# Optimization experiments

Measured on AMD Instinct MI355X. Metric: run time of the kernel, lower is better.

The kernel has to match this reference:

```python
import jax, jax.numpy as jnp
import numpy as np

N_NODES = 50000
N_EDGES = 600000
D_IN = 128
D_HID = 128
D_OUT = 40
EPS = 1e-5


def setup_inputs() -> dict:
    key = jax.random.key(0)
    ks = jax.random.split(key, 16)
    inp = {
        "x": jax.random.normal(ks[0], (N_NODES, D_IN), dtype=jnp.float32),
        "edge_index": jax.random.randint(ks[1], (2, N_EDGES), 0, N_NODES, dtype=jnp.int64),
    }
    dims = [(D_IN, D_HID), (D_HID, D_HID), (D_HID, D_OUT)]
    for i, (di, do) in enumerate(dims):
        s = 1.0 / np.sqrt(di)
        inp[f"W_l{i}"] = jax.random.uniform(ks[2 + 3 * i], (di, do), jnp.float32, -s, s)
        inp[f"b_l{i}"] = jax.random.uniform(ks[3 + 3 * i], (do,), jnp.float32, -s, s)
        inp[f"W_r{i}"] = jax.random.uniform(ks[4 + 3 * i], (di, do), jnp.float32, -s, s)
    for i in range(2):  # num_convs - 1 Trans (LayerNorm) blocks
        inp[f"g{i}"] = jnp.ones((D_HID,), jnp.float32)
        inp[f"be{i}"] = jnp.zeros((D_HID,), jnp.float32)
    return inp


def _sage_conv(x, src, dst, W_l, b_l, W_r):
    # mean-aggregate neighbor features at dst, then lin_l(agg) + lin_r(x)
    msg = jax.ops.segment_sum(x[src], dst, num_segments=N_NODES)  # [N, d]
    deg = jax.ops.segment_sum(jnp.ones((src.shape[0],), x.dtype), dst, num_segments=N_NODES)
    agg = msg / jnp.clip(deg, 1.0)[:, None]
    return agg @ W_l + b_l + x @ W_r


def _trans(x, g, b):
    # LayerNorm -> GELU (exact); Dropout p=0 is identity
    mu = jnp.mean(x, axis=-1, keepdims=True)
    var = jnp.mean(jnp.square(x - mu), axis=-1, keepdims=True)
    xn = (x - mu) * jax.lax.rsqrt(var + EPS) * g + b
    return jax.nn.gelu(xn, approximate=False)


def reference(x, edge_index, W_l0, b_l0, W_r0, W_l1, b_l1, W_r1, W_l2, b_l2, W_r2, g0, be0, g1, be1):
    src, dst = edge_index[0], edge_index[1]
    h = _sage_conv(x, src, dst, W_l0, b_l0, W_r0)
    h = _sage_conv(_trans(h, g0, be0), src, dst, W_l1, b_l1, W_r1)
    h = _sage_conv(_trans(h, g1, be1), src, dst, W_l2, b_l2, W_r2)
    return jax.nn.log_softmax(h, axis=1)
```

## Files before the change

kernel.cpp:

```cpp
#include <hip/hip_runtime.h>
#include <math.h>

#define N_NODES 50000
#define N_EDGES 600000
#define DF 128
#define KK 256
#define DOUT 40
#define EPSN 1e-5f
#define NB1 196

typedef __attribute__((ext_vector_type(8))) short sh8;
typedef __attribute__((ext_vector_type(4))) float f32x4;

__device__ __forceinline__ unsigned short f2b(float f) {
  unsigned u = __builtin_bit_cast(unsigned, f);
  unsigned r = u + 0x7FFFu + ((u >> 16) & 1u);
  return (unsigned short)(r >> 16);
}
__device__ __forceinline__ float b2f(unsigned short b) {
  unsigned u = ((unsigned)b) << 16;
  return __builtin_bit_cast(float, u);
}

__global__ __launch_bounds__(256) void k_count(
    const int* __restrict__ ei, int* __restrict__ counts) {
  int e = blockIdx.x * 256 + threadIdx.x;
  if (e < N_EDGES) atomicAdd(&counts[ei[N_EDGES + e]], 1);
}

__global__ __launch_bounds__(256) void k_bsum(
    const int* __restrict__ counts, int* __restrict__ bsum) {
  int i = blockIdx.x * 256 + threadIdx.x;
  int v = (i < N_NODES) ? counts[i] : 0;
  #pragma unroll
  for (int m = 1; m < 64; m <<= 1) v += __shfl_xor(v, m);
  __shared__ int ws[4];
  if ((threadIdx.x & 63) == 0) ws[threadIdx.x >> 6] = v;
  __syncthreads();
  if (threadIdx.x == 0) bsum[blockIdx.x] = ws[0] + ws[1] + ws[2] + ws[3];
}

__global__ __launch_bounds__(256) void k_bscan(
    const int* __restrict__ bsum, int* __restrict__ bbase) {
  const int t = threadIdx.x, lane = t & 63, w = t >> 6;
  int v = (t < NB1) ? bsum[t] : 0;
  int s = v;
  #pragma unroll
  for (int off = 1; off < 64; off <<= 1) {
    int u = __shfl_up(s, off);
    if (lane >= off) s += u;
  }
  __shared__ int wtot[4];
  if (lane == 63) wtot[w] = s;
  __syncthreads();
  int add = 0;
  for (int k = 0; k < w; ++k) add += wtot[k];
  if (t < NB1) bbase[t] = s + add - v;
}

__global__ __launch_bounds__(256) void k_rowptr(
    const int* __restrict__ counts, const int* __restrict__ bbase,
    int* __restrict__ rowptr, int* __restrict__ cursor,
    float* __restrict__ invdeg) {
  const int i = blockIdx.x * 256 + threadIdx.x;
  const int lane = threadIdx.x & 63, w = threadIdx.x >> 6;
  int c = (i < N_NODES) ? counts[i] : 0;
  int s = c;
  #pragma unroll
  for (int off = 1; off < 64; off <<= 1) {
    int u = __shfl_up(s, off);
    if (lane >= off) s += u;
  }
  __shared__ int wtot[4];
  if (lane == 63) wtot[w] = s;
  __syncthreads();
  int add = bbase[blockIdx.x];
  for (int k = 0; k < w; ++k) add += wtot[k];
  if (i < N_NODES) {
    int excl = s - c + add;
    rowptr[i] = excl;
    cursor[i] = excl;
    invdeg[i] = 1.0f / (float)((c > 1) ? c : 1);
  }
  if (i == 0) rowptr[N_NODES] = N_EDGES;
}

__global__ __launch_bounds__(256) void k_fill(
    const int* __restrict__ ei, int* __restrict__ cursor, int* __restrict__ csr) {
  int e = blockIdx.x * 256 + threadIdx.x;
  if (e < N_EDGES) {
    int d = ei[N_EDGES + e];
    int p = atomicAdd(&cursor[d], 1);
    csr[p] = ei[e];
  }
}

__global__ __launch_bounds__(256) void k_cvt_x(
    const float* __restrict__ x, unsigned* __restrict__ A) {
  int i = blockIdx.x * 256 + threadIdx.x;
  if (i >= N_NODES * 64) return;
  int n = i >> 6, p = i & 63;
  float2 v = ((const float2*)x)[i];
  A[(size_t)n * 128 + 64 + p] = (unsigned)f2b(v.x) | ((unsigned)f2b(v.y) << 16);
}

__global__ __launch_bounds__(256) void k_cvt_w(
    const float* __restrict__ Wl, const float* __restrict__ Wr,
    unsigned short* __restrict__ WT, int Nact, int total) {
  int i = blockIdx.x * 256 + threadIdx.x;
  if (i >= total) return;
  int n = i >> 8, k = i & 255;
  float v = 0.0f;
  if (n < Nact) v = (k < DF) ? Wl[k * Nact + n] : Wr[(k - DF) * Nact + n];
  WT[i] = f2b(v);
}

__global__ __launch_bounds__(256) void k_agg(
    unsigned* __restrict__ A, const int* __restrict__ rowptr,
    const int* __restrict__ csr, const float* __restrict__ invdeg) {
  const int node = (blockIdx.x * 256 + threadIdx.x) >> 6;
  const int lane = threadIdx.x & 63;
  if (node >= N_NODES) return;
  const int beg = rowptr[node], end = rowptr[node + 1];
  float ax = 0.f, ay = 0.f, bx = 0.f, by = 0.f;
  float cx = 0.f, cy = 0.f, dx = 0.f, dy = 0.f;
  int j = beg;
  for (; j + 4 <= end; j += 4) {
    int c0 = csr[j], c1 = csr[j + 1], c2 = csr[j + 2], c3 = csr[j + 3];
    unsigned p0 = A[(size_t)c0 * 128 + 64 + lane];
    unsigned p1 = A[(size_t)c1 * 128 + 64 + lane];
    unsigned p2 = A[(size_t)c2 * 128 + 64 + lane];
    unsigned p3 = A[(size_t)c3 * 128 + 64 + lane];
    ax += b2f((unsigned short)p0); ay += b2f((unsigned short)(p0 >> 16));
    bx += b2f((unsigned short)p1); by += b2f((unsigned short)(p1 >> 16));
    cx += b2f((unsigned short)p2); cy += b2f((unsigned short)(p2 >> 16));
    dx += b2f((unsigned short)p3); dy += b2f((unsigned short)(p3 >> 16));
  }
  for (; j < end; ++j) {
    unsigned p = A[(size_t)csr[j] * 128 + 64 + lane];
    ax += b2f((unsigned short)p); ay += b2f((unsigned short)(p >> 16));
  }
  ax += bx + cx + dx;
  ay += by + cy + dy;
  const float rd = invdeg[node];
  A[(size_t)node * 128 + lane] =
      (unsigned)f2b(ax * rd) | ((unsigned)f2b(ay * rd) << 16);
}

__global__ __launch_bounds__(256) void k_gemm128(
    const unsigned short* __restrict__ Acat, const unsigned short* __restrict__ WT,
    const float* __restrict__ bl, const float* __restrict__ g,
    const float* __restrict__ be, unsigned short* __restrict__ Adst) {
  __shared__ unsigned short Wlds[128 * KK];
  const int t = threadIdx.x;
  #pragma unroll
  for (int it = 0; it < 16; ++it) {
    int c = it * 256 + t;
    int n = c >> 5, k16 = c & 31;
    sh8 v = *(const sh8*)(WT + (size_t)n * KK + k16 * 8);
    unsigned off = (unsigned)((n * 512 + k16 * 16) ^ ((n & 7) << 4));
    *(sh8*)((char*)Wlds + off) = v;
  }
  __syncthreads();

  const int wave = t >> 6, lane = t & 63;
  const int lr = lane & 15, lg = lane >> 4;
  const int rw = blockIdx.x * 128 + wave * 32;

  sh8 a[2][8];
  #pragma unroll
  for (int rf = 0; rf < 2; ++rf) {
    int arow = rw + rf * 16 + lr;
    if (arow >= N_NODES) arow = N_NODES - 1;
    const sh8* Ap = (const sh8*)(Acat + (size_t)arow * KK + lg * 8);
    #pragma unroll
    for (int ks = 0; ks < 8; ++ks) a[rf][ks] = Ap[ks * 4];
  }

  f32x4 accs[2][8];
  #pragma unroll
  for (int rf = 0; rf < 2; ++rf)
    #pragma unroll
    for (int f = 0; f < 8; ++f) accs[rf][f] = (f32x4){0.f, 0.f, 0.f, 0.f};

  #pragma unroll
  for (int f = 0; f < 8; ++f) {
    const int n = f * 16 + lr;
    const unsigned swz = (unsigned)((n & 7) << 4);
    #pragma unroll
    for (int ks = 0; ks < 8; ++ks) {
      unsigned off = (unsigned)(n * 512 + ks * 64 + lg * 16) ^ swz;
      sh8 b = *(const sh8*)((const char*)Wlds + off);
      accs[0][f] = __builtin_amdgcn_mfma_f32_16x16x32_bf16(a[0][ks], b, accs[0][f], 0, 0, 0);
      accs[1][f] = __builtin_amdgcn_mfma_f32_16x16x32_bf16(a[1][ks], b, accs[1][f], 0, 0, 0);
    }
  }

  #pragma unroll
  for (int rf = 0; rf < 2; ++rf) {
    float s[4] = {0, 0, 0, 0}, sq[4] = {0, 0, 0, 0};
    #pragma unroll
    for (int f = 0; f < 8; ++f) {
      float bc = bl[lr + 16 * f];
      #pragma unroll
      for (int r = 0; r < 4; ++r) {
        float v = accs[rf][f][r] + bc;
        accs[rf][f][r] = v;
        s[r] += v; sq[r] += v * v;
      }
    }
    #pragma unroll
    for (int m = 1; m < 16; m <<= 1) {
      #pragma unroll
      for (int r = 0; r < 4; ++r) {
        s[r]  += __shfl_xor(s[r], m);
        sq[r] += __shfl_xor(sq[r], m);
      }
    }
    #pragma unroll
    for (int r = 0; r < 4; ++r) {
      float mu = s[r] * (1.0f / 128.0f);
      float var = sq[r] * (1.0f / 128.0f) - mu * mu;
      float rs = rsqrtf(var + EPSN);
      s[r] = mu; sq[r] = rs;
    }
    #pragma unroll
    for (int f = 0; f < 8; ++f) {
      float gv = g[lr + 16 * f], bev = be[lr + 16 * f];
      #pragma unroll
      for (int r = 0; r < 4; ++r) {
        int row = rw + rf * 16 + lg * 4 + r;
        float xn = (accs[rf][f][r] - s[r]) * sq[r] * gv + bev;
        float gel = 0.5f * xn * (1.0f + erff(xn * 0.70710678118654752f));
        if (row < N_NODES)
          Adst[(size_t)row * KK + 128 + lr + 16 * f] = f2b(gel);
      }
    }
  }
}

__global__ __launch_bounds__(256) void k_gemm40(
    const unsigned short* __restrict__ Acat, const unsigned short* __restrict__ WT,
    const float* __restrict__ bl, float* __restrict__ out) {
  __shared__ unsigned short Wlds[48 * KK];
  const int t = threadIdx.x;
  #pragma unroll
  for (int it = 0; it < 6; ++it) {
    int c = it * 256 + t;
    int n = c >> 5, k16 = c & 31;
    sh8 v = *(const sh8*)(WT + (size_t)n * KK + k16 * 8);
    unsigned off = (unsigned)((n * 512 + k16 * 16) ^ ((n & 7) << 4));
    *(sh8*)((char*)Wlds + off) = v;
  }
  __syncthreads();

  const int wave = t >> 6, lane = t & 63;
  const int lr = lane & 15, lg = lane >> 4;
  const int rw = blockIdx.x * 128 + wave * 32;

  sh8 a[2][8];
  #pragma unroll
  for (int rf = 0; rf < 2; ++rf) {
    int arow = rw + rf * 16 + lr;
    if (arow >= N_NODES) arow = N_NODES - 1;
    const sh8* Ap = (const sh8*)(Acat + (size_t)arow * KK + lg * 8);
    #pragma unroll
    for (int ks = 0; ks < 8; ++ks) a[rf][ks] = Ap[ks * 4];
  }

  f32x4 accs[2][3];
  #pragma unroll
  for (int rf = 0; rf < 2; ++rf)
    #pragma unroll
    for (int f = 0; f < 3; ++f) accs[rf][f] = (f32x4){0.f, 0.f, 0.f, 0.f};

  #pragma unroll
  for (int f = 0; f < 3; ++f) {
    const int n = f * 16 + lr;
    const unsigned swz = (unsigned)((n & 7) << 4);
    #pragma unroll
    for (int ks = 0; ks < 8; ++ks) {
      unsigned off = (unsigned)(n * 512 + ks * 64 + lg * 16) ^ swz;
      sh8 b = *(const sh8*)((const char*)Wlds + off);
      accs[0][f] = __builtin_amdgcn_mfma_f32_16x16x32_bf16(a[0][ks], b, accs[0][f], 0, 0, 0);
      accs[1][f] = __builtin_amdgcn_mfma_f32_16x16x32_bf16(a[1][ks], b, accs[1][f], 0, 0, 0);
    }
  }

  const bool v2 = (lr < 8);
  #pragma unroll
  for (int rf = 0; rf < 2; ++rf) {
    float vals[3][4];
    #pragma unroll
    for (int f = 0; f < 3; ++f) {
      int col = lr + 16 * f;
      float bc = (col < DOUT) ? bl[col] : 0.0f;
      #pragma unroll
      for (int r = 0; r < 4; ++r) vals[f][r] = accs[rf][f][r] + bc;
    }
    #pragma unroll
    for (int r = 0; r < 4; ++r) {
      float m = fmaxf(vals[0][r], vals[1][r]);
      if (v2) m = fmaxf(m, vals[2][r]);
      #pragma unroll
      for (int k = 1; k < 16; k <<= 1) m = fmaxf(m, __shfl_xor(m, k));
      float se = expf(vals[0][r] - m) + expf(vals[1][r] - m) +
                 (v2 ? expf(vals[2][r] - m) : 0.0f);
      #pragma unroll
      for (int k = 1; k < 16; k <<= 1) se += __shfl_xor(se, k);
      float lse = m + logf(se);
      int row = rw + rf * 16 + lg * 4 + r;
      if (row < N_NODES) {
        out[(size_t)row * DOUT + lr]      = vals[0][r] - lse;
        out[(size_t)row * DOUT + 16 + lr] = vals[1][r] - lse;
        if (v2) out[(size_t)row * DOUT + 32 + lr] = vals[2][r] - lse;
      }
    }
  }
}

extern "C" void kernel_launch(void* const* d_in, const int* in_sizes, int n_in,
                              void* d_out, int out_size, void* d_ws, size_t ws_size,
                              hipStream_t stream) {
  const float* x   = (const float*)d_in[0];
  const int*   ei  = (const int*)d_in[1];
  const float* Wl0 = (const float*)d_in[2];
  const float* bl0 = (const float*)d_in[3];
  const float* Wr0 = (const float*)d_in[4];
  const float* Wl1 = (const float*)d_in[5];
  const float* bl1 = (const float*)d_in[6];
  const float* Wr1 = (const float*)d_in[7];
  const float* Wl2 = (const float*)d_in[8];
  const float* bl2 = (const float*)d_in[9];
  const float* Wr2 = (const float*)d_in[10];
  const float* g0  = (const float*)d_in[11];
  const float* be0 = (const float*)d_in[12];
  const float* g1  = (const float*)d_in[13];
  const float* be1 = (const float*)d_in[14];
  float* out = (float*)d_out;

  unsigned short* A   = (unsigned short*)d_ws;
  unsigned short* WT0 = A + (size_t)N_NODES * KK;
  unsigned short* WT1 = WT0 + 128 * KK;
  unsigned short* WT2 = WT1 + 128 * KK;
  float* invdeg = (float*)(WT2 + 48 * KK);
  int*   counts = (int*)(invdeg + N_NODES);
  int*   rowptr = counts + N_NODES;
  int*   cursor = rowptr + N_NODES + 1;
  int*   csr    = cursor + N_NODES;
  int*   bsum   = csr + N_EDGES;
  int*   bbase  = bsum + NB1;

  const int egrid = (N_EDGES + 255) / 256;
  const int xgrid = (N_NODES * 64) / 256;
  const int agrid = (N_NODES * 64) / 256;
  const int ggrid = (N_NODES + 127) / 128;

  hipMemsetAsync(counts, 0, N_NODES * sizeof(int), stream);
  k_count<<<egrid, 256, 0, stream>>>(ei, counts);
  k_bsum<<<NB1, 256, 0, stream>>>(counts, bsum);
  k_bscan<<<1, 256, 0, stream>>>(bsum, bbase);
  k_rowptr<<<NB1, 256, 0, stream>>>(counts, bbase, rowptr, cursor, invdeg);
  k_fill<<<egrid, 256, 0, stream>>>(ei, cursor, csr);

  k_cvt_x<<<xgrid, 256, 0, stream>>>(x, (unsigned*)A);
  k_cvt_w<<<128, 256, 0, stream>>>(Wl0, Wr0, WT0, 128, 128 * KK);
  k_cvt_w<<<128, 256, 0, stream>>>(Wl1, Wr1, WT1, 128, 128 * KK);
  k_cvt_w<<<48, 256, 0, stream>>>(Wl2, Wr2, WT2, DOUT, 48 * KK);

  k_agg<<<agrid, 256, 0, stream>>>((unsigned*)A, rowptr, csr, invdeg);
  k_gemm128<<<ggrid, 256, 0, stream>>>(A, WT0, bl0, g0, be0, A);

  k_agg<<<agrid, 256, 0, stream>>>((unsigned*)A, rowptr, csr, invdeg);
  k_gemm128<<<ggrid, 256, 0, stream>>>(A, WT1, bl1, g1, be1, A);

  k_agg<<<agrid, 256, 0, stream>>>((unsigned*)A, rowptr, csr, invdeg);
  k_gemm40<<<ggrid, 256, 0, stream>>>(A, WT2, bl2, out);
}
```

Before: 243.1 us.

## Restructure GEMM kernels: stage A tile in LDS, keep weights in registers, coalesce stores

Both GEMM kernels now process 64 rows per block. The activation tile is staged in swizzled LDS and each wave keeps its slice of the weight columns in registers, rather than every block loading the full weight matrix into LDS. The LayerNorm row statistics are reduced across waves through a small LDS buffer. Outputs are written to LDS first and then stored to global memory with coalesced 16-byte writes. This aims to cut redundant weight staging and scattered 2-byte stores, at the cost of extra barriers and twice as many blocks.

```diff
diff --git a/kernel.cpp b/kernel.cpp
--- a/kernel.cpp
+++ b/kernel.cpp
@@ -151,90 +151,109 @@
     const unsigned short* __restrict__ Acat, const unsigned short* __restrict__ WT,
     const float* __restrict__ bl, const float* __restrict__ g,
     const float* __restrict__ be, unsigned short* __restrict__ Adst) {
-  __shared__ unsigned short Wlds[128 * KK];
+  __shared__ __align__(16) char lds[34816];
+  unsigned short* olds = (unsigned short*)lds;
+  float2* pp = (float2*)(lds + 32768);
+
   const int t = threadIdx.x;
-  #pragma unroll
-  for (int it = 0; it < 16; ++it) {
-    int c = it * 256 + t;
-    int n = c >> 5, k16 = c & 31;
-    sh8 v = *(const sh8*)(WT + (size_t)n * KK + k16 * 8);
-    unsigned off = (unsigned)((n * 512 + k16 * 16) ^ ((n & 7) << 4));
-    *(sh8*)((char*)Wlds + off) = v;
-  }
-  __syncthreads();
-
+  const int rw = blockIdx.x * 64;
   const int wave = t >> 6, lane = t & 63;
   const int lr = lane & 15, lg = lane >> 4;
-  const int rw = blockIdx.x * 128 + wave * 32;
-
-  sh8 a[2][8];
-  #pragma unroll
-  for (int rf = 0; rf < 2; ++rf) {
-    int arow = rw + rf * 16 + lr;
-    if (arow >= N_NODES) arow = N_NODES - 1;
-    const sh8* Ap = (const sh8*)(Acat + (size_t)arow * KK + lg * 8);
-    #pragma unroll
-    for (int ks = 0; ks < 8; ++ks) a[rf][ks] = Ap[ks * 4];
-  }
-
-  f32x4 accs[2][8];
-  #pragma unroll
-  for (int rf = 0; rf < 2; ++rf)
-    #pragma unroll
-    for (int f = 0; f < 8; ++f) accs[rf][f] = (f32x4){0.f, 0.f, 0.f, 0.f};
-
-  #pragma unroll
-  for (int f = 0; f < 8; ++f) {
-    const int n = f * 16 + lr;
-    const unsigned swz = (unsigned)((n & 7) << 4);
-    #pragma unroll
-    for (int ks = 0; ks < 8; ++ks) {
-      unsigned off = (unsigned)(n * 512 + ks * 64 + lg * 16) ^ swz;
-      sh8 b = *(const sh8*)((const char*)Wlds + off);
-      accs[0][f] = __builtin_amdgcn_mfma_f32_16x16x32_bf16(a[0][ks], b, accs[0][f], 0, 0, 0);
-      accs[1][f] = __builtin_amdgcn_mfma_f32_16x16x32_bf16(a[1][ks], b, accs[1][f], 0, 0, 0);
-    }
-  }
-
-  #pragma unroll
-  for (int rf = 0; rf < 2; ++rf) {
-    float s[4] = {0, 0, 0, 0}, sq[4] = {0, 0, 0, 0};
-    #pragma unroll
-    for (int f = 0; f < 8; ++f) {
-      float bc = bl[lr + 16 * f];
-      #pragma unroll
-      for (int r = 0; r < 4; ++r) {
-        float v = accs[rf][f][r] + bc;
-        accs[rf][f][r] = v;
-        s[r] += v; sq[r] += v * v;
-      }
+
+  #pragma unroll
+  for (int it = 0; it < 8; ++it) {
+    int id = it * 256 + t;
+    int r = id >> 5, c = id & 31;
+    int gr = rw + r; if (gr >= N_NODES) gr = N_NODES - 1;
+    sh8 v = *(const sh8*)(Acat + (size_t)gr * KK + c * 8);
+    unsigned off = (unsigned)((r * 512 + c * 16) ^ ((r & 7) << 4));
+    *(sh8*)(lds + off) = v;
+  }
+
+  sh8 Bfrag[2][8];
+  #pragma unroll
+  for (int fl = 0; fl < 2; ++fl) {
+    const int n = wave * 32 + fl * 16 + lr;
+    const sh8* Bp = (const sh8*)(WT + (size_t)n * KK + lg * 8);
+    #pragma unroll
+    for (int ks = 0; ks < 8; ++ks) Bfrag[fl][ks] = Bp[ks * 4];
+  }
+  const int col0 = wave * 32 + lr, col1 = col0 + 16;
+  const float bc0 = bl[col0], bc1 = bl[col1];
+  const float gv0 = g[col0], gv1 = g[col1];
+  const float bev0 = be[col0], bev1 = be[col1];
+
+  __syncthreads();
+
+  f32x4 accs[4][2];
+  #pragma unroll
+  for (int rf = 0; rf < 4; ++rf)
+    #pragma unroll
+    for (int fl = 0; fl < 2; ++fl) accs[rf][fl] = (f32x4){0.f, 0.f, 0.f, 0.f};
+
+  #pragma unroll
+  for (int ks = 0; ks < 8; ++ks) {
+    #pragma unroll
+    for (int rf = 0; rf < 4; ++rf) {
+      const int r = rf * 16 + lr;
+      unsigned off = (unsigned)((r * 512 + ks * 64 + lg * 16) ^ ((r & 7) << 4));
+      sh8 a = *(const sh8*)(lds + off);
+      accs[rf][0] = __builtin_amdgcn_mfma_f32_16x16x32_bf16(a, Bfrag[0][ks], accs[rf][0], 0, 0, 0);
+      accs[rf][1] = __builtin_amdgcn_mfma_f32_16x16x32_bf16(a, Bfrag[1][ks], accs[rf][1], 0, 0, 0);
+    }
+  }
+
+  #pragma unroll
+  for (int rf = 0; rf < 4; ++rf) {
+    float sv[4], qv[4];
+    #pragma unroll
+    for (int r = 0; r < 4; ++r) {
+      float v0 = accs[rf][0][r] + bc0;
+      float v1 = accs[rf][1][r] + bc1;
+      accs[rf][0][r] = v0; accs[rf][1][r] = v1;
+      sv[r] = v0 + v1; qv[r] = v0 * v0 + v1 * v1;
     }
     #pragma unroll
     for (int m = 1; m < 16; m <<= 1) {
       #pragma unroll
       for (int r = 0; r < 4; ++r) {
-        s[r]  += __shfl_xor(s[r], m);
-        sq[r] += __shfl_xor(sq[r], m);
+        sv[r] += __shfl_xor(sv[r], m);
+        qv[r] += __shfl_xor(qv[r], m);
       }
     }
+    if (lr == 0) {
+      #pragma unroll
+      for (int r = 0; r < 4; ++r)
+        pp[wave * 64 + rf * 16 + lg * 4 + r] = make_float2(sv[r], qv[r]);
+    }
+  }
+  __syncthreads();
+
+  #pragma unroll
+  for (int rf = 0; rf < 4; ++rf) {
     #pragma unroll
     for (int r = 0; r < 4; ++r) {
-      float mu = s[r] * (1.0f / 128.0f);
-      float var = sq[r] * (1.0f / 128.0f) - mu * mu;
+      const int row = rf * 16 + lg * 4 + r;
+      float2 q0 = pp[row], q1 = pp[64 + row], q2 = pp[128 + row], q3 = pp[192 + row];
+      float mu = (q0.x + q1.x + q2.x + q3.x) * (1.0f / 128.0f);
+      float var = (q0.y + q1.y + q2.y + q3.y) * (1.0f / 128.0f) - mu * mu;
       float rs = rsqrtf(var + EPSN);
-      s[r] = mu; sq[r] = rs;
-    }
-    #pragma unroll
-    for (int f = 0; f < 8; ++f) {
-      float gv = g[lr + 16 * f], bev = be[lr + 16 * f];
-      #pragma unroll
-      for (int r = 0; r < 4; ++r) {
-        int row = rw + rf * 16 + lg * 4 + r;
-        float xn = (accs[rf][f][r] - s[r]) * sq[r] * gv + bev;
-        float gel = 0.5f * xn * (1.0f + erff(xn * 0.70710678118654752f));
-        if (row < N_NODES)
-          Adst[(size_t)row * KK + 128 + lr + 16 * f] = f2b(gel);
-      }
+      float xn0 = (accs[rf][0][r] - mu) * rs * gv0 + bev0;
+      float xn1 = (accs[rf][1][r] - mu) * rs * gv1 + bev1;
+      olds[row * 136 + col0] = f2b(0.5f * xn0 * (1.0f + erff(xn0 * 0.70710678118654752f)));
+      olds[row * 136 + col1] = f2b(0.5f * xn1 * (1.0f + erff(xn1 * 0.70710678118654752f)));
+    }
+  }
+  __syncthreads();
+
+  #pragma unroll
+  for (int it = 0; it < 4; ++it) {
+    int id = it * 256 + t;
+    int r = id >> 4, c = id & 15;
+    int gr = rw + r;
+    if (gr < N_NODES) {
+      sh8 v = *(const sh8*)((char*)olds + r * 272 + c * 16);
+      *(sh8*)(Adst + (size_t)gr * KK + 128 + c * 8) = v;
     }
   }
 }
@@ -242,79 +261,86 @@
 __global__ __launch_bounds__(256) void k_gemm40(
     const unsigned short* __restrict__ Acat, const unsigned short* __restrict__ WT,
     const float* __restrict__ bl, float* __restrict__ out) {
-  __shared__ unsigned short Wlds[48 * KK];
+  __shared__ __align__(16) char lds[43008];
+  float* folds = (float*)(lds + 32768);
+
   const int t = threadIdx.x;
-  #pragma unroll
-  for (int it = 0; it < 6; ++it) {
-    int c = it * 256 + t;
-    int n = c >> 5, k16 = c & 31;
-    sh8 v = *(const sh8*)(WT + (size_t)n * KK + k16 * 8);
-    unsigned off = (unsigned)((n * 512 + k16 * 16) ^ ((n & 7) << 4));
-    *(sh8*)((char*)Wlds + off) = v;
-  }
-  __syncthreads();
-
+  const int rw = blockIdx.x * 64;
   const int wave = t >> 6, lane = t & 63;
   const int lr = lane & 15, lg = lane >> 4;
-  const int rw = blockIdx.x * 128 + wave * 32;
-
-  sh8 a[2][8];
-  #pragma unroll
-  for (int rf = 0; rf < 2; ++rf) {
-    int arow = rw + rf * 16 + lr;
-    if (arow >= N_NODES) arow = N_NODES - 1;
-    const sh8* Ap = (const sh8*)(Acat + (size_t)arow * KK + lg * 8);
-    #pragma unroll
-    for (int ks = 0; ks < 8; ++ks) a[rf][ks] = Ap[ks * 4];
-  }
-
-  f32x4 accs[2][3];
-  #pragma unroll
-  for (int rf = 0; rf < 2; ++rf)
-    #pragma unroll
-    for (int f = 0; f < 3; ++f) accs[rf][f] = (f32x4){0.f, 0.f, 0.f, 0.f};
-
+
+  #pragma unroll
+  for (int it = 0; it < 8; ++it) {
+    int id = it * 256 + t;
+    int r = id >> 5, c = id & 31;
+    int gr = rw + r; if (gr >= N_NODES) gr = N_NODES - 1;
+    sh8 v = *(const sh8*)(Acat + (size_t)gr * KK + c * 8);
+    unsigned off = (unsigned)((r * 512 + c * 16) ^ ((r & 7) << 4));
+    *(sh8*)(lds + off) = v;
+  }
+
+  sh8 Bfrag[3][8];
   #pragma unroll
   for (int f = 0; f < 3; ++f) {
     const int n = f * 16 + lr;
-    const unsigned swz = (unsigned)((n & 7) << 4);
-    #pragma unroll
-    for (int ks = 0; ks < 8; ++ks) {
-      unsigned off = (unsigned)(n * 512 + ks * 64 + lg * 16) ^ swz;
-      sh8 b = *(const sh8*)((const char*)Wlds + off);
-      accs[0][f] = __builtin_amdgcn_mfma_f32_16x16x32_bf16(a[0][ks], b, accs[0][f], 0, 0, 0);
-      accs[1][f] = __builtin_amdgcn_mfma_f32_16x16x32_bf16(a[1][ks], b, accs[1][f], 0, 0, 0);
-    }
+    const sh8* Bp = (const sh8*)(WT + (size_t)n * KK + lg * 8);
+    #pragma unroll
+    for (int ks = 0; ks < 8; ++ks) Bfrag[f][ks] = Bp[ks * 4];
+  }
+
+  __syncthreads();
+
+  f32x4 accs[3];
+  #pragma unroll
+  for (int f = 0; f < 3; ++f) accs[f] = (f32x4){0.f, 0.f, 0.f, 0.f};
+
+  #pragma unroll
+  for (int ks = 0; ks < 8; ++ks) {
+    const int r = wave * 16 + lr;
+    unsigned off = (unsigned)((r * 512 + ks * 64 + lg * 16) ^ ((r & 7) << 4));
+    sh8 a = *(const sh8*)(lds + off);
+    #pragma unroll
+    for (int f = 0; f < 3; ++f)
+      accs[f] = __builtin_amdgcn_mfma_f32_16x16x32_bf16(a, Bfrag[f][ks], accs[f], 0, 0, 0);
   }
 
   const bool v2 = (lr < 8);
-  #pragma unroll
-  for (int rf = 0; rf < 2; ++rf) {
-    float vals[3][4];
-    #pragma unroll
-    for (int f = 0; f < 3; ++f) {
-      int col = lr + 16 * f;
-      float bc = (col < DOUT) ? bl[col] : 0.0f;
-      #pragma unroll
-      for (int r = 0; r < 4; ++r) vals[f][r] = accs[rf][f][r] + bc;
-    }
-    #pragma unroll
-    for (int r = 0; r < 4; ++r) {
-      float m = fmaxf(vals[0][r], vals[1][r]);
-      if (v2) m = fmaxf(m, vals[2][r]);
-      #pragma unroll
-      for (int k = 1; k < 16; k <<= 1) m = fmaxf(m, __shfl_xor(m, k));
-      float se = expf(vals[0][r] - m) + expf(vals[1][r] - m) +
-                 (v2 ? expf(vals[2][r] - m) : 0.0f);
-      #pragma unroll
-      for (int k = 1; k < 16; k <<= 1) se += __shfl_xor(se, k);
-      float lse = m + logf(se);
-      int row = rw + rf * 16 + lg * 4 + r;
-      if (row < N_NODES) {
-        out[(size_t)row * DOUT + lr]      = vals[0][r] - lse;
-        out[(size_t)row * DOUT + 16 + lr] = vals[1][r] - lse;
-        if (v2) out[(size_t)row * DOUT + 32 + lr] = vals[2][r] - lse;
-      }
+  float vals[3][4];
+  #pragma unroll
+  for (int f = 0; f < 3; ++f) {
+    int col = lr + 16 * f;
+    float bc = (col < DOUT) ? bl[col] : 0.0f;
+    #pragma unroll
+    for (int r = 0; r < 4; ++r) vals[f][r] = accs[f][r] + bc;
+  }
+  #pragma unroll
+  for (int r = 0; r < 4; ++r) {
+    float m = fmaxf(vals[0][r], vals[1][r]);
+    if (v2) m = fmaxf(m, vals[2][r]);
+    #pragma unroll
+    for (int k = 1; k < 16; k <<= 1) m = fmaxf(m, __shfl_xor(m, k));
+    float se = expf(vals[0][r] - m) + expf(vals[1][r] - m) +
+               (v2 ? expf(vals[2][r] - m) : 0.0f);
+    #pragma unroll
+    for (int k = 1; k < 16; k <<= 1) se += __shfl_xor(se, k);
+    float lse = m + logf(se);
+    const int row = wave * 16 + lg * 4 + r;
+    folds[row * 40 + lr]      = vals[0][r] - lse;
+    folds[row * 40 + 16 + lr] = vals[1][r] - lse;
+    if (v2) folds[row * 40 + 32 + lr] = vals[2][r] - lse;
+  }
+  __syncthreads();
+
+  #pragma unroll
+  for (int it = 0; it < 3; ++it) {
+    int id = it * 256 + t;
+    if (id < 640) {
+      int r = (id * 6554) >> 16;
+      int c = id - r * 10;
+      int gr = rw + r;
+      if (gr < N_NODES)
+        *(float4*)(out + (size_t)gr * DOUT + c * 4) =
+            *(const float4*)(folds + r * 40 + c * 4);
     }
   }
 }
@@ -354,7 +380,7 @@
   const int egrid = (N_EDGES + 255) / 256;
   const int xgrid = (N_NODES * 64) / 256;
   const int agrid = (N_NODES * 64) / 256;
-  const int ggrid = (N_NODES + 127) / 128;
+  const int ggrid = (N_NODES + 63) / 64;
 
   hipMemsetAsync(counts, 0, N_NODES * sizeof(int), stream);
   k_count<<<egrid, 256, 0, stream>>>(ei, counts);
```

Measured after the change: 253.2 us. 1.04x slower.
